# Kernel optimization log

Hardware: AMD Instinct MI355X
Metric: run time of the kernel (lower is better)

## Reference

```python
import jax, jax.numpy as jnp
import numpy as np
from jax import lax


def _conv3x3_same(x, w):
    # x: [N,C,H,W], w: [O,I,3,3], padding=1, stride=1, no bias
    return lax.conv_general_dilated(
        x, w, window_strides=(1, 1), padding=((1, 1), (1, 1)),
        dimension_numbers=("NCHW", "OIHW", "NCHW"))


def _maxpool2x2(x):
    return lax.reduce_window(x, -jnp.inf, lax.max,
                             window_dimensions=(1, 1, 2, 2),
                             window_strides=(1, 1, 2, 2),
                             padding="VALID")


def setup_inputs() -> dict:
    key = jax.random.key(0)
    k1, k2, k3 = jax.random.split(key, 3)
    H = 4096
    W = 4096
    x = jax.random.normal(k1, (2, 1, H, W), dtype=jnp.float32)
    W1 = jax.random.normal(k2, (1, 1, 3, 3), dtype=jnp.float32)
    W2 = jax.random.normal(k3, (1, 1, 3, 3), dtype=jnp.float32)
    return {"x": x, "W1": W1, "W2": W2, "H": H, "W": W, "nTh": 4, "nTw": 4}


def reference(x, W1, W2, H, W, nTh, nTw):
    # Tiled execution in the original is math-equivalent to the full pipeline:
    # conv3x3(same) -> maxpool2x2 -> conv3x3(same) -> maxpool2x2
    h1 = _conv3x3_same(x, W1)
    h2 = _maxpool2x2(h1)          # [N,C,H/2,W/2]
    h3 = _conv3x3_same(h2, W2)
    out = _maxpool2x2(h3)         # [N,C,H/4,W/4]
    return out
```

## Files before the change

### kernel.cpp

```cpp
#include <hip/hip_runtime.h>


#define HIMG 4096
#define ODIM 1024
#define H2W  2048
#define DOUT 8
#define SHROWS 18
#define SHSTR 2052

__global__ __launch_bounds__(1024, 4)
void fused_net(const float* __restrict__ x, const float* __restrict__ W1,
               const float* __restrict__ W2, float* __restrict__ out)
{
    __shared__ float h2s[SHROWS][SHSTR];

    const int tid  = threadIdx.x;
    const int lane = tid & 63;
    const int o0   = blockIdx.x * DOUT;
    const int img  = blockIdx.y;
    const long xoff = (long)img * HIMG * HIMG;

    float w1[9], w2[9];
#pragma unroll
    for (int i = 0; i < 9; ++i) { w1[i] = W1[i]; w2[i] = W2[i]; }

    if (tid < SHROWS)                   h2s[tid][1]       = 0.f;
    if (tid >= 64 && tid < 64 + SHROWS) h2s[tid - 64][2050] = 0.f;

    float accA[4] = {0.f, 0.f, 0.f, 0.f};
    float accB[4] = {0.f, 0.f, 0.f, 0.f};
    const int xr0 = 4 * o0 - 3;
    const int x0  = 4 * tid;

    auto rowA = [&](int t, float (&dd)[4]) {
        const int gy = xr0 + t;
        float4 v = make_float4(0.f, 0.f, 0.f, 0.f);
        float xl = 0.f, xr = 0.f;
        if ((unsigned)gy < (unsigned)HIMG) {
            const float* xrow = x + xoff + (long)gy * HIMG;
            v  = *(const float4*)(xrow + x0);
            xl = __shfl_up(v.w, 1);
            xr = __shfl_down(v.x, 1);
            if (lane == 0)  xl = (tid > 0)    ? xrow[x0 - 1] : 0.f;
            if (lane == 63) xr = (tid < 1023) ? xrow[x0 + 4] : 0.f;
        }
        const float xv[6] = {xl, v.x, v.y, v.z, v.w, xr};
#pragma unroll
        for (int j = 0; j < 4; ++j) {
            float d = accA[j];
            d = fmaf(w1[6], xv[j], d); d = fmaf(w1[7], xv[j+1], d); d = fmaf(w1[8], xv[j+2], d);
            float a = accB[j];
            a = fmaf(w1[3], xv[j], a); a = fmaf(w1[4], xv[j+1], a); a = fmaf(w1[5], xv[j+2], a);
            float b = w1[0] * xv[j];
            b = fmaf(w1[1], xv[j+1], b); b = fmaf(w1[2], xv[j+2], b);
            dd[j] = d; accA[j] = a; accB[j] = b;
        }
    };

    float stash[4], done[4];
    rowA(0, done);
    rowA(1, done);
#pragma unroll 2
    for (int tp = 1; tp < 19; ++tp) {
        rowA(2 * tp,     stash);
        rowA(2 * tp + 1, done);
        const int srow = tp - 1;
        const int Pg = 2 * o0 - 1 + srow;
        float2 hv;
        hv.x = fmaxf(fmaxf(stash[0], stash[1]), fmaxf(done[0], done[1]));
        hv.y = fmaxf(fmaxf(stash[2], stash[3]), fmaxf(done[2], done[3]));
        if ((unsigned)Pg >= (unsigned)H2W) hv = make_float2(0.f, 0.f);
        *(float2*)&h2s[srow][2 * tid + 2] = hv;
    }

    __syncthreads();

    float dA[2] = {0.f, 0.f}, dB[2] = {0.f, 0.f};
    auto rowB = [&](int R, float (&dd)[2]) {
        const float* rp = &h2s[R][2 * tid + 1];
        const float s1 = rp[0], s2 = rp[1], s3 = rp[2], s4 = rp[3];
        float d0 = dA[0];
        d0 = fmaf(w2[6], s1, d0); d0 = fmaf(w2[7], s2, d0); d0 = fmaf(w2[8], s3, d0);
        float a0 = dB[0];
        a0 = fmaf(w2[3], s1, a0); a0 = fmaf(w2[4], s2, a0); a0 = fmaf(w2[5], s3, a0);
        float b0 = w2[0] * s1; b0 = fmaf(w2[1], s2, b0); b0 = fmaf(w2[2], s3, b0);
        dd[0] = d0; dA[0] = a0; dB[0] = b0;
        float d1 = dA[1];
        d1 = fmaf(w2[6], s2, d1); d1 = fmaf(w2[7], s3, d1); d1 = fmaf(w2[8], s4, d1);
        float a1 = dB[1];
        a1 = fmaf(w2[3], s2, a1); a1 = fmaf(w2[4], s3, a1); a1 = fmaf(w2[5], s4, a1);
        float b1 = w2[0] * s2; b1 = fmaf(w2[1], s3, b1); b1 = fmaf(w2[2], s4, b1);
        dd[1] = d1; dA[1] = a1; dB[1] = b1;
    };

    float dst[2], ddn[2];
    rowB(0, ddn);
    rowB(1, ddn);
    const long obase = (long)img * ODIM * ODIM;
#pragma unroll
    for (int rp2 = 1; rp2 < 9; ++rp2) {
        rowB(2 * rp2,     dst);
        rowB(2 * rp2 + 1, ddn);
        const float res = fmaxf(fmaxf(dst[0], dst[1]), fmaxf(ddn[0], ddn[1]));
        out[obase + (long)(o0 + rp2 - 1) * ODIM + tid] = res;
    }
}

extern "C" void kernel_launch(void* const* d_in, const int* in_sizes, int n_in,
                              void* d_out, int out_size, void* d_ws, size_t ws_size,
                              hipStream_t stream) {
    const float* x  = (const float*)d_in[0];
    const float* W1 = (const float*)d_in[1];
    const float* W2 = (const float*)d_in[2];
    float* out = (float*)d_out;

    dim3 grid(ODIM / DOUT, 2);
    fused_net<<<grid, dim3(1024), 0, stream>>>(x, W1, W2, out);
}
```

Baseline: 212.2 us.

## Replace shared-memory staging with register-streamed fused conv using shuffles and halo lanes

New measurement: 261.5 us. 1.23x slower.

```diff
diff --git a/kernel.cpp b/kernel.cpp
--- a/kernel.cpp
+++ b/kernel.cpp
@@ -4,46 +4,57 @@
 #define HIMG 4096
 #define ODIM 1024
 #define H2W  2048
-#define DOUT 8
-#define SHROWS 18
-#define SHSTR 2052
 
-__global__ __launch_bounds__(1024, 4)
-void fused_net(const float* __restrict__ x, const float* __restrict__ W1,
-               const float* __restrict__ W2, float* __restrict__ out)
+__global__ __launch_bounds__(256, 8)
+void fused_net_v4(const float* __restrict__ x, const float* __restrict__ W1,
+                  const float* __restrict__ W2, float* __restrict__ out)
 {
-    __shared__ float h2s[SHROWS][SHSTR];
+    const int id  = blockIdx.x;
+    const int nid = (id & 7) * 256 + (id >> 3);
+    const int img    = nid >> 10;
+    const int rr     = nid & 1023;
+    const int band   = rr >> 2;
+    const int colseg = rr & 3;
 
     const int tid  = threadIdx.x;
     const int lane = tid & 63;
-    const int o0   = blockIdx.x * DOUT;
-    const int img  = blockIdx.y;
+    const int oc   = (colseg << 8) + tid;
+    const int o0   = band << 2;
+    const int x0   = oc << 2;
     const long xoff = (long)img * HIMG * HIMG;
 
     float w1[9], w2[9];
 #pragma unroll
     for (int i = 0; i < 9; ++i) { w1[i] = W1[i]; w2[i] = W2[i]; }
 
-    if (tid < SHROWS)                   h2s[tid][1]       = 0.f;
-    if (tid >= 64 && tid < 64 + SHROWS) h2s[tid - 64][2050] = 0.f;
+    const bool haloL = (lane == 0);
+    const bool haloR = (lane == 63);
+    const bool halo  = haloL | haloR;
+    const bool hvalid = haloL ? (oc > 0) : (oc < ODIM - 1);
+    int hx = haloL ? x0 - 4 : x0 + 4;
+    if (hx < 0) hx = 0;
+    if (hx > HIMG - 4) hx = HIMG - 4;
 
-    float accA[4] = {0.f, 0.f, 0.f, 0.f};
-    float accB[4] = {0.f, 0.f, 0.f, 0.f};
-    const int xr0 = 4 * o0 - 3;
-    const int x0  = 4 * tid;
+    const int xr0 = (o0 << 2) - 3;
 
-    auto rowA = [&](int t, float (&dd)[4]) {
+    float accA[4] = {0,0,0,0}, accB[4] = {0,0,0,0};
+    float accAh[2] = {0,0}, accBh[2] = {0,0};
+    float dA[2] = {0,0}, dB[2] = {0,0};
+    float p0 = 0.f, p1 = 0.f;
+
+    auto rowA = [&](int t, float (&dd)[4], float (&ddh)[2]) {
         const int gy = xr0 + t;
-        float4 v = make_float4(0.f, 0.f, 0.f, 0.f);
-        float xl = 0.f, xr = 0.f;
+        float4 v  = make_float4(0.f, 0.f, 0.f, 0.f);
+        float4 vh = make_float4(0.f, 0.f, 0.f, 0.f);
         if ((unsigned)gy < (unsigned)HIMG) {
             const float* xrow = x + xoff + (long)gy * HIMG;
-            v  = *(const float4*)(xrow + x0);
-            xl = __shfl_up(v.w, 1);
-            xr = __shfl_down(v.x, 1);
-            if (lane == 0)  xl = (tid > 0)    ? xrow[x0 - 1] : 0.f;
-            if (lane == 63) xr = (tid < 1023) ? xrow[x0 + 4] : 0.f;
+            v = *(const float4*)(xrow + x0);
+            if (halo) vh = *(const float4*)(xrow + hx);
         }
+        float xl = __shfl_up(v.w, 1);
+        float xr = __shfl_down(v.x, 1);
+        if (haloL) xl = hvalid ? vh.w : 0.f;
+        if (haloR) xr = hvalid ? vh.x : 0.f;
         const float xv[6] = {xl, v.x, v.y, v.z, v.w, xr};
 #pragma unroll
         for (int j = 0; j < 4; ++j) {
@@ -55,54 +66,69 @@
             b = fmaf(w1[1], xv[j+1], b); b = fmaf(w1[2], xv[j+2], b);
             dd[j] = d; accA[j] = a; accB[j] = b;
         }
+        if (halo) {
+            const float t0 = haloL ? vh.y : v.w;
+            const float t1 = haloL ? vh.z : vh.x;
+            const float t2 = haloL ? vh.w : vh.y;
+            const float t3 = haloL ? v.x  : vh.z;
+            const float hv4[4] = {t0, t1, t2, t3};
+#pragma unroll
+            for (int j = 0; j < 2; ++j) {
+                float d = accAh[j];
+                d = fmaf(w1[6], hv4[j], d); d = fmaf(w1[7], hv4[j+1], d); d = fmaf(w1[8], hv4[j+2], d);
+                float a = accBh[j];
+                a = fmaf(w1[3], hv4[j], a); a = fmaf(w1[4], hv4[j+1], a); a = fmaf(w1[5], hv4[j+2], a);
+                float b = w1[0] * hv4[j];
+                b = fmaf(w1[1], hv4[j+1], b); b = fmaf(w1[2], hv4[j+2], b);
+                ddh[j] = d; accAh[j] = a; accBh[j] = b;
+            }
+        }
     };
 
-    float stash[4], done[4];
-    rowA(0, done);
-    rowA(1, done);
+    float dd0[4], dd1[4], ddh0[2], ddh1[2];
+    rowA(0, dd0, ddh0);
+    rowA(1, dd0, ddh0);
+
+    const long obase = (long)img * ODIM * ODIM + oc;
+
 #pragma unroll 2
-    for (int tp = 1; tp < 19; ++tp) {
-        rowA(2 * tp,     stash);
-        rowA(2 * tp + 1, done);
-        const int srow = tp - 1;
-        const int Pg = 2 * o0 - 1 + srow;
-        float2 hv;
-        hv.x = fmaxf(fmaxf(stash[0], stash[1]), fmaxf(done[0], done[1]));
-        hv.y = fmaxf(fmaxf(stash[2], stash[3]), fmaxf(done[2], done[3]));
-        if ((unsigned)Pg >= (unsigned)H2W) hv = make_float2(0.f, 0.f);
-        *(float2*)&h2s[srow][2 * tid + 2] = hv;
-    }
+    for (int s = 0; s < 10; ++s) {
+        rowA(2 * s + 2, dd0, ddh0);
+        rowA(2 * s + 3, dd1, ddh1);
 
-    __syncthreads();
+        float hvx = fmaxf(fmaxf(dd0[0], dd0[1]), fmaxf(dd1[0], dd1[1]));
+        float hvy = fmaxf(fmaxf(dd0[2], dd0[3]), fmaxf(dd1[2], dd1[3]));
+        float hh  = fmaxf(fmaxf(ddh0[0], ddh0[1]), fmaxf(ddh1[0], ddh1[1]));
+        const int P = 2 * o0 - 1 + s;
+        const bool pok = (unsigned)P < (unsigned)H2W;
+        if (!pok) { hvx = 0.f; hvy = 0.f; }
+        if (!pok || !hvalid) hh = 0.f;
 
-    float dA[2] = {0.f, 0.f}, dB[2] = {0.f, 0.f};
-    auto rowB = [&](int R, float (&dd)[2]) {
-        const float* rp = &h2s[R][2 * tid + 1];
-        const float s1 = rp[0], s2 = rp[1], s3 = rp[2], s4 = rp[3];
-        float d0 = dA[0];
-        d0 = fmaf(w2[6], s1, d0); d0 = fmaf(w2[7], s2, d0); d0 = fmaf(w2[8], s3, d0);
+        const float su = __shfl_up(hvy, 1);
+        const float sd = __shfl_down(hvx, 1);
+        const float s1 = haloL ? hh : su;
+        const float s4 = haloR ? hh : sd;
+
+        float e0 = dA[0];
+        e0 = fmaf(w2[6], s1, e0); e0 = fmaf(w2[7], hvx, e0); e0 = fmaf(w2[8], hvy, e0);
         float a0 = dB[0];
-        a0 = fmaf(w2[3], s1, a0); a0 = fmaf(w2[4], s2, a0); a0 = fmaf(w2[5], s3, a0);
-        float b0 = w2[0] * s1; b0 = fmaf(w2[1], s2, b0); b0 = fmaf(w2[2], s3, b0);
-        dd[0] = d0; dA[0] = a0; dB[0] = b0;
-        float d1 = dA[1];
-        d1 = fmaf(w2[6], s2, d1); d1 = fmaf(w2[7], s3, d1); d1 = fmaf(w2[8], s4, d1);
+        a0 = fmaf(w2[3], s1, a0); a0 = fmaf(w2[4], hvx, a0); a0 = fmaf(w2[5], hvy, a0);
+        float b0 = w2[0] * s1;  b0 = fmaf(w2[1], hvx, b0); b0 = fmaf(w2[2], hvy, b0);
+        float e1 = dA[1];
+        e1 = fmaf(w2[6], hvx, e1); e1 = fmaf(w2[7], hvy, e1); e1 = fmaf(w2[8], s4, e1);
         float a1 = dB[1];
-        a1 = fmaf(w2[3], s2, a1); a1 = fmaf(w2[4], s3, a1); a1 = fmaf(w2[5], s4, a1);
-        float b1 = w2[0] * s2; b1 = fmaf(w2[1], s3, b1); b1 = fmaf(w2[2], s4, b1);
-        dd[1] = d1; dA[1] = a1; dB[1] = b1;
-    };
+        a1 = fmaf(w2[3], hvx, a1); a1 = fmaf(w2[4], hvy, a1); a1 = fmaf(w2[5], s4, a1);
+        float b1 = w2[0] * hvx; b1 = fmaf(w2[1], hvy, b1); b1 = fmaf(w2[2], s4, b1);
+        dA[0] = a0; dB[0] = b0; dA[1] = a1; dB[1] = b1;
 
-    float dst[2], ddn[2];
-    rowB(0, ddn);
-    rowB(1, ddn);
-    const long obase = (long)img * ODIM * ODIM;
-#pragma unroll
-    for (int rp2 = 1; rp2 < 9; ++rp2) {
-        rowB(2 * rp2,     dst);
-        rowB(2 * rp2 + 1, ddn);
-        const float res = fmaxf(fmaxf(dst[0], dst[1]), fmaxf(ddn[0], ddn[1]));
-        out[obase + (long)(o0 + rp2 - 1) * ODIM + tid] = res;
+        if (s >= 2) {
+            if (s & 1) {
+                const float res = fmaxf(fmaxf(p0, p1), fmaxf(e0, e1));
+                out[obase + (long)(o0 + ((s - 3) >> 1)) * ODIM] = res;
+            } else {
+                p0 = e0; p1 = e1;
+            }
+        }
     }
 }
 
@@ -114,6 +140,5 @@
     const float* W2 = (const float*)d_in[2];
     float* out = (float*)d_out;
 
-    dim3 grid(ODIM / DOUT, 2);
-    fused_net<<<grid, dim3(1024), 0, stream>>>(x, W1, W2, out);
+    fused_net_v4<<<dim3(2048), dim3(256), 0, stream>>>(x, W1, W2, out);
 }
```
